# Kernel tuning notes

Measured on AMD Instinct MI355X. Metric: run time of the kernel, lower is better.

## Reference

```python
import jax, jax.numpy as jnp
import numpy as np

T, K, N = 4096, 4096, 11008  # tokens, in_features, out_features


def _unpack_int4(packed):
    """packed: int8 [..., K//2] -> signed 4-bit values int8 [..., K].
    Low nibble first, high nibble second; arithmetic shifts sign-extend."""
    lo = jnp.right_shift(jnp.left_shift(packed, 4).astype(jnp.int8), 4)
    hi = jnp.right_shift(packed, 4).astype(jnp.int8)
    out = jnp.stack([lo, hi], axis=-1)  # [..., K//2, 2]
    return out.reshape(*packed.shape[:-1], packed.shape[-1] * 2)


def _pack_int4(vals):
    """vals: int8 in [-8,7], [..., K] -> packed int8 [..., K//2]."""
    v = vals.reshape(*vals.shape[:-1], vals.shape[-1] // 2, 2)
    lo = v[..., 0] & 0xF
    hi = v[..., 1] & 0xF
    return (lo | jnp.left_shift(hi, 4)).astype(jnp.int8)


def setup_inputs() -> dict:
    key = jax.random.key(0)
    k1, k2, k3, k4 = jax.random.split(key, 4)
    # symmetric 4-bit quantized values in [-7, 7], packed two per byte
    x_int = jax.random.randint(k1, (T, K), -7, 8).astype(jnp.int8)
    w_int = jax.random.randint(k2, (N, K), -7, 8).astype(jnp.int8)
    pq_x = _pack_int4(x_int)
    weight = _pack_int4(w_int)
    # per-token / per-output-channel dequant scales (max_abs/7 style magnitudes)
    scales_x = (jax.random.uniform(k3, (T,), jnp.float32) * 0.01 + 1e-4)
    weight_scales = (jax.random.uniform(k4, (N,), jnp.float32) * 0.01 + 1e-4)
    return {"pq_x": pq_x, "scales_x": scales_x, "weight": weight,
            "weight_scales": weight_scales}


def reference(pq_x, scales_x, weight, weight_scales):
    # Unpack int4 operands. Products |a*w| <= 49 and K=4096 => |acc| <= 2e5,
    # exactly representable in fp32, so the fp32 matmul equals int32 GEMM.
    a = _unpack_int4(pq_x).astype(jnp.float32)      # [T, K]
    w = _unpack_int4(weight).astype(jnp.float32)    # [N, K]
    acc = jnp.einsum('tk,nk->tn', a, w)             # integer GEMM in fp32
    # fused per-token x per-output-channel dequant
    out = acc * scales_x[:, None] * weight_scales[None, :]
    out = out.astype(jnp.float16)
    return out[None]  # unsqueeze(0) as in the torch module
```

## Files before the change

### kernel.cpp

```cpp
#include <hip/hip_runtime.h>
#include <hip/hip_fp16.h>
#include <stdint.h>


#define T_DIM 4096
#define K_DIM 4096
#define N_DIM 11008
#define KP    2048
#define BM 128
#define BN 256
#define STAGES 64
#define A_PANELS (T_DIM / BM)
#define B_PANELS (N_DIM / BN)
#define CHUNK_A 8192
#define CHUNK_B 16384
#define WS_A ((size_t)A_PANELS * STAGES * CHUNK_A)
#define WS_B ((size_t)B_PANELS * STAGES * CHUNK_B)
#define NA_BYTES ((size_t)T_DIM * KP)
#define NW_BYTES ((size_t)N_DIM * KP)

typedef __attribute__((ext_vector_type(4)))  int int32x4;
typedef __attribute__((ext_vector_type(16))) int int32x16;
typedef __attribute__((ext_vector_type(4)))  float floatx4;
typedef __attribute__((ext_vector_type(8)))  _Float16 f16x8;
typedef __attribute__((ext_vector_type(2)))  _Float16 f16x2;

__device__ __forceinline__ uint32_t pack4(int4 v) {
  return (uint32_t)(v.x & 0xFF) | ((uint32_t)(v.y & 0xFF) << 8) |
         ((uint32_t)(v.z & 0xFF) << 16) | ((uint32_t)(v.w & 0xFF) << 24);
}
__device__ __forceinline__ uint32_t nib_lo_s8(uint32_t p) {
  uint32_t t = (p & 0x0F0F0F0Fu) ^ 0x88888888u;
  return (t - 0x08080808u) ^ 0x80808080u;
}
__device__ __forceinline__ uint32_t nib_hi_s8(uint32_t p) {
  uint32_t t = ((p >> 4) & 0x0F0F0F0Fu) ^ 0x88888888u;
  return (t - 0x08080808u) ^ 0x80808080u;
}

__global__ __launch_bounds__(256) void unpack_tiles2(
    const int* __restrict__ xa, const int* __restrict__ xw,
    uint8_t* __restrict__ wsa, uint8_t* __restrict__ wsb)
{
  const int s  = blockIdx.x;
  const int yb = blockIdx.y;
  const int t  = threadIdx.x;
  const int r  = t >> 1, h = t & 1;

  const int* src; uint8_t* dst; int cellStride;
  if (yb < A_PANELS) {
    src = xa + ((size_t)(yb * 128 + r)) * KP + s * 32 + h * 16;
    dst = wsa + ((size_t)yb * STAGES + s) * CHUNK_A + r * 16;
    cellStride = 2048;
  } else {
    const int yb2 = yb - A_PANELS;
    const int panel = yb2 >> 1;
    const int rip = (yb2 & 1) * 128 + r;
    src = xw + ((size_t)(yb2 * 128 + r)) * KP + s * 32 + h * 16;
    dst = wsb + ((size_t)panel * STAGES + s) * CHUNK_B + rip * 16;
    cellStride = 4096;
  }
  const int4* s4 = (const int4*)src;
  const int4 v0 = s4[0], v1 = s4[1], v2 = s4[2], v3 = s4[3];
  const uint32_t b0 = pack4(v0), b1 = pack4(v1);
  const uint32_t b2 = pack4(v2), b3 = pack4(v3);
  uint4 o01, o23;
  o01.x = nib_lo_s8(b0); o01.y = nib_hi_s8(b0);
  o01.z = nib_lo_s8(b1); o01.w = nib_hi_s8(b1);
  o23.x = nib_lo_s8(b2); o23.y = nib_hi_s8(b2);
  o23.z = nib_lo_s8(b3); o23.w = nib_hi_s8(b3);
  *(uint4*)(dst + (2 * h    ) * cellStride) = o01;
  *(uint4*)(dst + (2 * h + 1) * cellStride) = o23;
}

__device__ __forceinline__ void dma16(const uint8_t* g, uint8_t* l) {
  __builtin_amdgcn_global_load_lds(
      (const __attribute__((address_space(1))) uint32_t*)g,
      (__attribute__((address_space(3))) uint32_t*)l, 16, 0, 0);
}

__global__ __launch_bounds__(256, 2) void gemm_i8_tb(
    const uint8_t* __restrict__ wsa, const uint8_t* __restrict__ wsb,
    const float* __restrict__ sx, const float* __restrict__ sw,
    float* __restrict__ out)
{
  __shared__ uint8_t sAmem[3 * CHUNK_A];
  __shared__ uint8_t sBmem[3 * CHUNK_B];

  const int tid  = threadIdx.x;
  const int lane = tid & 63;
  const int wv   = tid >> 6;
  const int wm   = wv >> 1, wn = wv & 1;
  const int h    = lane >> 5;
  const int ml   = lane & 31;
  const int pp   = blockIdx.x;
  const int qq   = blockIdx.y;

  const uint8_t* chunkA = wsa + (size_t)pp * STAGES * CHUNK_A;
  const uint8_t* chunkB = wsb + (size_t)qq * STAGES * CHUNK_B;
  const int segOff = wv * 1024 + lane * 16;
  const int ldsOff = wv * 1024;

  const int rowA = (wm * 64 + ml) * 16;
  const int rowB = (wn * 128 + ml) * 16;

  int32x16 acc[2][4];
#pragma unroll
  for (int mi = 0; mi < 2; ++mi)
#pragma unroll
    for (int ni = 0; ni < 4; ++ni)
#pragma unroll
      for (int i = 0; i < 16; ++i) acc[mi][ni][i] = 0;

  auto dma_stage = [&](int s, int buf) {
    const uint8_t* ca = chunkA + (size_t)s * CHUNK_A;
    const uint8_t* cb = chunkB + (size_t)s * CHUNK_B;
    uint8_t* la = sAmem + buf * CHUNK_A + ldsOff;
    uint8_t* lb = sBmem + buf * CHUNK_B + ldsOff;
#pragma unroll
    for (int i = 0; i < 2; ++i)
      dma16(ca + segOff + i * 4096, la + i * 4096);
#pragma unroll
    for (int i = 0; i < 4; ++i)
      dma16(cb + segOff + i * 4096, lb + i * 4096);
  };

  dma_stage(0, 0);
  dma_stage(1, 1);

  int rb = 0;
  int wb = 2;
#pragma unroll 1
  for (int s = 0; s < STAGES; ++s) {
    if (s < STAGES - 1) asm volatile("s_waitcnt vmcnt(6)" ::: "memory");
    else                asm volatile("s_waitcnt vmcnt(0)" ::: "memory");
    __builtin_amdgcn_s_barrier();
    if (s + 2 < STAGES) dma_stage(s + 2, wb);

    const uint8_t* baseA = sAmem + rb * CHUNK_A;
    const uint8_t* baseB = sBmem + rb * CHUNK_B;
#pragma unroll
    for (int s2 = 0; s2 < 2; ++s2) {
      const int c = 2 * s2 + h;
      const uint8_t* pa = baseA + c * 2048 + rowA;
      const uint8_t* pb = baseB + c * 4096 + rowB;
      int32x4 aF[2], bF[4];
#pragma unroll
      for (int mi = 0; mi < 2; ++mi) aF[mi] = *(const int32x4*)(pa + mi * 512);
#pragma unroll
      for (int ni = 0; ni < 4; ++ni) bF[ni] = *(const int32x4*)(pb + ni * 512);
#pragma unroll
      for (int mi = 0; mi < 2; ++mi)
#pragma unroll
        for (int ni = 0; ni < 4; ++ni)
          acc[mi][ni] = __builtin_amdgcn_mfma_i32_32x32x32_i8(
              aF[mi], bF[ni], acc[mi][ni], 0, 0, 0);
    }
    rb = (rb == 2) ? 0 : rb + 1;
    wb = (wb == 2) ? 0 : wb + 1;
  }

#pragma unroll
  for (int mi = 0; mi < 2; ++mi) {
    const int rbase = pp * BM + wm * 64 + mi * 32 + 4 * h;
    float sxv[16];
#pragma unroll
    for (int r = 0; r < 16; ++r) sxv[r] = sx[rbase + (r & 3) + 8 * (r >> 2)];
#pragma unroll
    for (int ni = 0; ni < 4; ++ni) {
      const int gcol = qq * BN + wn * 128 + ni * 32 + ml;
      const float swv = sw[gcol];
#pragma unroll
      for (int r = 0; r < 16; ++r) {
        const int grow = rbase + (r & 3) + 8 * (r >> 2);
        const float v = (float)acc[mi][ni][r] * sxv[r] * swv;
        out[(size_t)grow * N_DIM + gcol] = __half2float(__float2half(v));
      }
    }
  }
}

__global__ __launch_bounds__(256) void repack_int32_to_bytes(
    const int* __restrict__ xa, const int* __restrict__ xw,
    uint32_t* __restrict__ da, uint32_t* __restrict__ dw)
{
  const size_t i = (size_t)blockIdx.x * blockDim.x + threadIdx.x;
  const size_t na4 = NA_BYTES / 4;
  const int4* src; uint32_t* dst; size_t off;
  if (i < na4) { src = (const int4*)xa; dst = da; off = i; }
  else         { src = (const int4*)xw; dst = dw; off = i - na4; }
  const int4 v = src[off];
  dst[off] = pack4(v);
}

__device__ __forceinline__ uint32_t cvt2(uint32_t m) {
  union U { uint32_t u; f16x2 h; } a, b, c;
  a.u = m ^ 0x64086408u; b.u = 0xE408E408u; c.h = a.h + b.h;
  return c.u;
}
__device__ __forceinline__ void unpack_cell(uint32_t* cell, uint32_t p) {
  cell[0] = cvt2( p        & 0x000F000Fu);
  cell[1] = cvt2((p >> 4)  & 0x000F000Fu);
  cell[2] = cvt2((p >> 8)  & 0x000F000Fu);
  cell[3] = cvt2((p >> 12) & 0x000F000Fu);
}

template <bool PACKED>
__global__ __launch_bounds__(256) void linear4bit_f16(
    const uint8_t* __restrict__ pqx, const float* __restrict__ sx,
    const uint8_t* __restrict__ wq,  const float* __restrict__ sw,
    const int* __restrict__ pqx32,   const int* __restrict__ wq32,
    float* __restrict__ out)
{
  __shared__ uint32_t sAf[8][128][4];
  __shared__ uint32_t sBf[8][128][4];
  const int tid = threadIdx.x, lane = tid & 63, wv = tid >> 6;
  const int wm = wv >> 1, wn = wv & 1, qd = lane >> 4, m16 = lane & 15;
  const int bm0 = blockIdx.x * 128, bn0 = blockIdx.y * 128;
  const int srow = tid >> 1, sh = tid & 1;
  const uint8_t* aPtr = pqx + (size_t)(bm0 + srow) * KP + sh * 16;
  const uint8_t* bPtr = wq  + (size_t)(bn0 + srow) * KP + sh * 16;
  const int* aPtr32 = pqx32 + (size_t)(bm0 + srow) * KP + sh * 16;
  const int* bPtr32 = wq32  + (size_t)(bn0 + srow) * KP + sh * 16;
  floatx4 acc[4][4];
#pragma unroll
  for (int mi = 0; mi < 4; ++mi)
#pragma unroll
    for (int ni = 0; ni < 4; ++ni)
#pragma unroll
      for (int r = 0; r < 4; ++r) acc[mi][ni][r] = 0.0f;
  uint4 ar, br;
  auto load_stage = [&](int s) {
    if (PACKED) {
      ar = *(const uint4*)(aPtr + (size_t)s * 32);
      br = *(const uint4*)(bPtr + (size_t)s * 32);
    } else {
      const int4* a4 = (const int4*)(aPtr32 + (size_t)s * 32);
      const int4* b4 = (const int4*)(bPtr32 + (size_t)s * 32);
      ar.x = pack4(a4[0]); ar.y = pack4(a4[1]); ar.z = pack4(a4[2]); ar.w = pack4(a4[3]);
      br.x = pack4(b4[0]); br.y = pack4(b4[1]); br.z = pack4(b4[2]); br.w = pack4(b4[3]);
    }
  };
  auto stage_to_lds = [&]() {
    uint32_t pa[4] = {ar.x, ar.y, ar.z, ar.w};
    uint32_t pb[4] = {br.x, br.y, br.z, br.w};
#pragma unroll
    for (int i = 0; i < 4; ++i) {
      unpack_cell(&sAf[4 * sh + i][srow][0], pa[i]);
      unpack_cell(&sBf[4 * sh + i][srow][0], pb[i]);
    }
  };
  load_stage(0); stage_to_lds();
#pragma unroll 1
  for (int s = 0; s < STAGES; ++s) {
    __syncthreads();
    if (s + 1 < STAGES) load_stage(s + 1);
#pragma unroll
    for (int s2 = 0; s2 < 2; ++s2) {
      f16x8 aF[4], bF[4];
#pragma unroll
      for (int mi = 0; mi < 4; ++mi)
        aF[mi] = *(const f16x8*)&sAf[4 * s2 + qd][wm * 64 + mi * 16 + m16][0];
#pragma unroll
      for (int ni = 0; ni < 4; ++ni)
        bF[ni] = *(const f16x8*)&sBf[4 * s2 + qd][wn * 64 + ni * 16 + m16][0];
#pragma unroll
      for (int mi = 0; mi < 4; ++mi)
#pragma unroll
        for (int ni = 0; ni < 4; ++ni)
          acc[mi][ni] = __builtin_amdgcn_mfma_f32_16x16x32_f16(aF[mi], bF[ni], acc[mi][ni], 0, 0, 0);
    }
    __syncthreads();
    if (s + 1 < STAGES) stage_to_lds();
  }
#pragma unroll
  for (int mi = 0; mi < 4; ++mi) {
    const int grow0 = bm0 + wm * 64 + mi * 16 + qd * 4;
    const float s0 = sx[grow0], s1 = sx[grow0 + 1], s2v = sx[grow0 + 2], s3 = sx[grow0 + 3];
#pragma unroll
    for (int ni = 0; ni < 4; ++ni) {
      const int gcol = bn0 + wn * 64 + ni * 16 + m16;
      const float swv = sw[gcol];
      const floatx4 a = acc[mi][ni];
      out[(size_t)(grow0 + 0) * N_DIM + gcol] = __half2float(__float2half(a[0] * s0 * swv));
      out[(size_t)(grow0 + 1) * N_DIM + gcol] = __half2float(__float2half(a[1] * s1 * swv));
      out[(size_t)(grow0 + 2) * N_DIM + gcol] = __half2float(__float2half(a[2] * s2v * swv));
      out[(size_t)(grow0 + 3) * N_DIM + gcol] = __half2float(__float2half(a[3] * s3 * swv));
    }
  }
}

extern "C" void kernel_launch(void* const* d_in, const int* in_sizes, int n_in,
                              void* d_out, int out_size, void* d_ws, size_t ws_size,
                              hipStream_t stream) {
  const int*   pqx32 = (const int*)d_in[0];
  const float* sxp   = (const float*)d_in[1];
  const int*   wq32  = (const int*)d_in[2];
  const float* swp   = (const float*)d_in[3];
  float* outp = (float*)d_out;

  if (ws_size >= WS_A + WS_B) {
    uint8_t* wsa = (uint8_t*)d_ws;
    uint8_t* wsb = wsa + WS_A;
    unpack_tiles2<<<dim3(STAGES, A_PANELS + N_DIM / 128), 256, 0, stream>>>(
        pqx32, wq32, wsa, wsb);
    gemm_i8_tb<<<dim3(A_PANELS, B_PANELS), 256, 0, stream>>>(wsa, wsb, sxp, swp, outp);
  } else if (ws_size >= NA_BYTES + NW_BYTES) {
    uint8_t* da = (uint8_t*)d_ws;
    uint8_t* dw = da + NA_BYTES;
    const size_t total4 = (NA_BYTES + NW_BYTES) / 4;
    repack_int32_to_bytes<<<(uint32_t)(total4 / 256), 256, 0, stream>>>(
        pqx32, wq32, (uint32_t*)da, (uint32_t*)dw);
    linear4bit_f16<true><<<dim3(T_DIM / 128, N_DIM / 128), 256, 0, stream>>>(
        da, sxp, dw, swp, nullptr, nullptr, outp);
  } else {
    linear4bit_f16<false><<<dim3(T_DIM / 128, N_DIM / 128), 256, 0, stream>>>(
        nullptr, sxp, nullptr, swp, pqx32, wq32, outp);
  }
}
```

Baseline: 475.7 us.

## Use 8-wave GEMM blocks and LDS-staged coalesced unpack kernel

The GEMM block grows from 4 to 8 waves, so each wave computes a 64x64 sub-tile instead of 64x128, with the DMA loads split across more waves and the vmcnt wait adjusted to match. MFMA issue is wrapped in s_setprio to favour the matrix instructions. The unpack kernel is rewritten to read rows coalesced, unpack nibbles into a swizzled LDS tile, and then write the staged chunk layout in contiguous 16-byte stores. The aim is more latency hiding and better global-memory coalescing, at the cost of fewer accumulator registers per wave and more LDS fragment reads per MFMA.

```diff
diff --git a/kernel.cpp b/kernel.cpp
--- a/kernel.cpp
+++ b/kernel.cpp
@@ -38,39 +38,59 @@
   return (t - 0x08080808u) ^ 0x80808080u;
 }
 
-__global__ __launch_bounds__(256) void unpack_tiles2(
+#define ROWS_PB 32
+#define SGRP    16
+
+__global__ __launch_bounds__(256) void unpack_tiles3(
     const int* __restrict__ xa, const int* __restrict__ xw,
     uint8_t* __restrict__ wsa, uint8_t* __restrict__ wsb)
 {
-  const int s  = blockIdx.x;
-  const int yb = blockIdx.y;
-  const int t  = threadIdx.x;
-  const int r  = t >> 1, h = t & 1;
-
-  const int* src; uint8_t* dst; int cellStride;
-  if (yb < A_PANELS) {
-    src = xa + ((size_t)(yb * 128 + r)) * KP + s * 32 + h * 16;
-    dst = wsa + ((size_t)yb * STAGES + s) * CHUNK_A + r * 16;
-    cellStride = 2048;
+  __shared__ __align__(16) uint32_t lds[8192];
+  const int sg  = blockIdx.x;
+  const int yb  = blockIdx.y;
+  const int tid = threadIdx.x;
+
+  const int* srcBase; uint8_t* dstBase; int cellStride, chunkStride;
+  if (yb < T_DIM / ROWS_PB) {
+    srcBase = xa + (size_t)yb * ROWS_PB * KP + sg * SGRP * 32;
+    dstBase = wsa + ((size_t)(yb >> 2) * STAGES + sg * SGRP) * CHUNK_A
+                  + (size_t)(yb & 3) * (ROWS_PB * 16);
+    cellStride = 2048; chunkStride = CHUNK_A;
   } else {
-    const int yb2 = yb - A_PANELS;
-    const int panel = yb2 >> 1;
-    const int rip = (yb2 & 1) * 128 + r;
-    src = xw + ((size_t)(yb2 * 128 + r)) * KP + s * 32 + h * 16;
-    dst = wsb + ((size_t)panel * STAGES + s) * CHUNK_B + rip * 16;
-    cellStride = 4096;
-  }
-  const int4* s4 = (const int4*)src;
-  const int4 v0 = s4[0], v1 = s4[1], v2 = s4[2], v3 = s4[3];
-  const uint32_t b0 = pack4(v0), b1 = pack4(v1);
-  const uint32_t b2 = pack4(v2), b3 = pack4(v3);
-  uint4 o01, o23;
-  o01.x = nib_lo_s8(b0); o01.y = nib_hi_s8(b0);
-  o01.z = nib_lo_s8(b1); o01.w = nib_hi_s8(b1);
-  o23.x = nib_lo_s8(b2); o23.y = nib_hi_s8(b2);
-  o23.z = nib_lo_s8(b3); o23.w = nib_hi_s8(b3);
-  *(uint4*)(dst + (2 * h    ) * cellStride) = o01;
-  *(uint4*)(dst + (2 * h + 1) * cellStride) = o23;
+    const int zb = yb - T_DIM / ROWS_PB;
+    srcBase = xw + (size_t)zb * ROWS_PB * KP + sg * SGRP * 32;
+    dstBase = wsb + ((size_t)(zb >> 3) * STAGES + sg * SGRP) * CHUNK_B
+                  + (size_t)(zb & 7) * (ROWS_PB * 16);
+    cellStride = 4096; chunkStride = CHUNK_B;
+  }
+
+  const int lq    = tid & 127;
+  const int rhalf = tid >> 7;
+  const int sl    = lq >> 3;
+  const int tg    = lq & 7;
+  const int cellL = (tg & 1) * 2;
+  const int dsl   = tg >> 1;
+#pragma unroll
+  for (int it = 0; it < 16; ++it) {
+    const int row = it * 2 + rhalf;
+    const int4 v = *(const int4*)(srcBase + (size_t)row * KP + lq * 4);
+    const uint32_t p = pack4(v);
+    const int sp = sl ^ (row & 7);
+    uint32_t* b = &lds[(((cellL * 32 + row) << 4) + sp) * 4 + dsl];
+    b[0]    = nib_lo_s8(p);
+    b[2048] = nib_hi_s8(p);
+  }
+  __syncthreads();
+
+  const int row2 = tid & 31;
+#pragma unroll
+  for (int it = 0; it < 8; ++it) {
+    const int pr = it * 8 + (tid >> 5);
+    const int s2 = pr >> 2, cl = pr & 3;
+    const int sp = s2 ^ (row2 & 7);
+    const uint4 v = *(const uint4*)&lds[(((cl * 32 + row2) << 4) + sp) * 4];
+    *(uint4*)(dstBase + (size_t)s2 * chunkStride + cl * cellStride + row2 * 16) = v;
+  }
 }
 
 __device__ __forceinline__ void dma16(const uint8_t* g, uint8_t* l) {
@@ -79,18 +99,18 @@
       (__attribute__((address_space(3))) uint32_t*)l, 16, 0, 0);
 }
 
-__global__ __launch_bounds__(256, 2) void gemm_i8_tb(
+__global__ __launch_bounds__(512, 4) void gemm_i8_tb2(
     const uint8_t* __restrict__ wsa, const uint8_t* __restrict__ wsb,
     const float* __restrict__ sx, const float* __restrict__ sw,
     float* __restrict__ out)
 {
-  __shared__ uint8_t sAmem[3 * CHUNK_A];
-  __shared__ uint8_t sBmem[3 * CHUNK_B];
+  __shared__ __align__(16) uint8_t sAmem[3 * CHUNK_A];
+  __shared__ __align__(16) uint8_t sBmem[3 * CHUNK_B];
 
   const int tid  = threadIdx.x;
   const int lane = tid & 63;
   const int wv   = tid >> 6;
-  const int wm   = wv >> 1, wn = wv & 1;
+  const int wm   = wv >> 2, wn = wv & 3;
   const int h    = lane >> 5;
   const int ml   = lane & 31;
   const int pp   = blockIdx.x;
@@ -98,31 +118,29 @@
 
   const uint8_t* chunkA = wsa + (size_t)pp * STAGES * CHUNK_A;
   const uint8_t* chunkB = wsb + (size_t)qq * STAGES * CHUNK_B;
-  const int segOff = wv * 1024 + lane * 16;
-  const int ldsOff = wv * 1024;
+  const int laneOff = lane * 16;
+  const int aOffW   = wv * 1024;
+  const int bOffW   = wv * 2048;
 
   const int rowA = (wm * 64 + ml) * 16;
-  const int rowB = (wn * 128 + ml) * 16;
-
-  int32x16 acc[2][4];
+  const int rowB = (wn * 64 + ml) * 16;
+
+  int32x16 acc[2][2];
 #pragma unroll
   for (int mi = 0; mi < 2; ++mi)
 #pragma unroll
-    for (int ni = 0; ni < 4; ++ni)
+    for (int ni = 0; ni < 2; ++ni)
 #pragma unroll
       for (int i = 0; i < 16; ++i) acc[mi][ni][i] = 0;
 
   auto dma_stage = [&](int s, int buf) {
     const uint8_t* ca = chunkA + (size_t)s * CHUNK_A;
     const uint8_t* cb = chunkB + (size_t)s * CHUNK_B;
-    uint8_t* la = sAmem + buf * CHUNK_A + ldsOff;
-    uint8_t* lb = sBmem + buf * CHUNK_B + ldsOff;
-#pragma unroll
-    for (int i = 0; i < 2; ++i)
-      dma16(ca + segOff + i * 4096, la + i * 4096);
-#pragma unroll
-    for (int i = 0; i < 4; ++i)
-      dma16(cb + segOff + i * 4096, lb + i * 4096);
+    uint8_t* la = sAmem + buf * CHUNK_A;
+    uint8_t* lb = sBmem + buf * CHUNK_B;
+    dma16(ca + aOffW + laneOff,        la + aOffW);
+    dma16(cb + bOffW + laneOff,        lb + bOffW);
+    dma16(cb + bOffW + 1024 + laneOff, lb + bOffW + 1024);
   };
 
   dma_stage(0, 0);
@@ -132,7 +150,7 @@
   int wb = 2;
 #pragma unroll 1
   for (int s = 0; s < STAGES; ++s) {
-    if (s < STAGES - 1) asm volatile("s_waitcnt vmcnt(6)" ::: "memory");
+    if (s < STAGES - 1) asm volatile("s_waitcnt vmcnt(3)" ::: "memory");
     else                asm volatile("s_waitcnt vmcnt(0)" ::: "memory");
     __builtin_amdgcn_s_barrier();
     if (s + 2 < STAGES) dma_stage(s + 2, wb);
@@ -144,17 +162,19 @@
       const int c = 2 * s2 + h;
       const uint8_t* pa = baseA + c * 2048 + rowA;
       const uint8_t* pb = baseB + c * 4096 + rowB;
-      int32x4 aF[2], bF[4];
+      int32x4 aF[2], bF[2];
 #pragma unroll
       for (int mi = 0; mi < 2; ++mi) aF[mi] = *(const int32x4*)(pa + mi * 512);
 #pragma unroll
-      for (int ni = 0; ni < 4; ++ni) bF[ni] = *(const int32x4*)(pb + ni * 512);
+      for (int ni = 0; ni < 2; ++ni) bF[ni] = *(const int32x4*)(pb + ni * 512);
+      __builtin_amdgcn_s_setprio(1);
 #pragma unroll
       for (int mi = 0; mi < 2; ++mi)
 #pragma unroll
-        for (int ni = 0; ni < 4; ++ni)
+        for (int ni = 0; ni < 2; ++ni)
           acc[mi][ni] = __builtin_amdgcn_mfma_i32_32x32x32_i8(
               aF[mi], bF[ni], acc[mi][ni], 0, 0, 0);
+      __builtin_amdgcn_s_setprio(0);
     }
     rb = (rb == 2) ? 0 : rb + 1;
     wb = (wb == 2) ? 0 : wb + 1;
@@ -167,8 +187,8 @@
 #pragma unroll
     for (int r = 0; r < 16; ++r) sxv[r] = sx[rbase + (r & 3) + 8 * (r >> 2)];
 #pragma unroll
-    for (int ni = 0; ni < 4; ++ni) {
-      const int gcol = qq * BN + wn * 128 + ni * 32 + ml;
+    for (int ni = 0; ni < 2; ++ni) {
+      const int gcol = qq * BN + wn * 64 + ni * 32 + ml;
       const float swv = sw[gcol];
 #pragma unroll
       for (int r = 0; r < 16; ++r) {
@@ -302,9 +322,9 @@
   if (ws_size >= WS_A + WS_B) {
     uint8_t* wsa = (uint8_t*)d_ws;
     uint8_t* wsb = wsa + WS_A;
-    unpack_tiles2<<<dim3(STAGES, A_PANELS + N_DIM / 128), 256, 0, stream>>>(
+    unpack_tiles3<<<dim3(STAGES / SGRP, T_DIM / ROWS_PB + N_DIM / ROWS_PB), 256, 0, stream>>>(
         pqx32, wq32, wsa, wsb);
-    gemm_i8_tb<<<dim3(A_PANELS, B_PANELS), 256, 0, stream>>>(wsa, wsb, sxp, swp, outp);
+    gemm_i8_tb2<<<dim3(A_PANELS, B_PANELS), 512, 0, stream>>>(wsa, wsb, sxp, swp, outp);
   } else if (ws_size >= NA_BYTES + NW_BYTES) {
     uint8_t* da = (uint8_t*)d_ws;
     uint8_t* dw = da + NA_BYTES;
```

Result: no change. 466.8 us (-1.9%).
